# Performance work log

Measured on AMD Instinct MI355X. Metric: run time of the kernel, lower is better.

Reference implementation:

```python
import jax, jax.numpy as jnp
import numpy as np

THRESH = 0.5
MARGIN = 0.1
SCALE_POS = 2.0
SCALE_NEG = 40.0
EPS = 1e-5


def setup_inputs() -> dict:
    key = jax.random.key(0)
    k1, k2 = jax.random.split(key)
    B, D, NUM_CLASSES = 4096, 512, 512
    feats = jax.random.normal(k1, (B, D), dtype=jnp.float32)
    feats = feats / jnp.linalg.norm(feats, axis=1, keepdims=True)  # unit-norm embeddings
    labels = jax.random.randint(k2, (B,), 0, NUM_CLASSES, dtype=jnp.int64)
    return {"feats": feats, "labels": labels, "label_num": 26}


def reference(feats, labels, label_num):
    B = feats.shape[0]
    sim = feats @ feats.T  # [B, B]
    same = labels[:, None] == labels[None, :]
    pos_m = same & (sim < 1.0 - EPS)      # pos_pair_ mask per row
    neg_m = ~same                         # neg_pair_ mask per row
    has_pos = pos_m.any(axis=1)
    has_neg = neg_m.any(axis=1)
    min_pos = jnp.min(jnp.where(pos_m, sim, jnp.inf), axis=1)
    max_neg = jnp.max(jnp.where(neg_m, sim, -jnp.inf), axis=1)
    pos_thr = jnp.where(has_pos, min_pos, jnp.float32(0.2))  # fallback when no pos pairs
    neg_thr = jnp.where(has_neg, max_neg, jnp.float32(0.8))  # fallback when no neg pairs
    # mined pairs (same semantics as the per-row boolean filtering)
    neg_pair = neg_m & (sim + MARGIN > pos_thr[:, None])
    pos_pair = pos_m & (sim - MARGIN < neg_thr[:, None])
    valid = pos_pair.any(axis=1) & neg_pair.any(axis=1) & (jnp.arange(B) < B - label_num)
    # masked log-sum-exp style reductions (exp of -inf on masked entries -> 0)
    pos_sum = jnp.sum(jnp.exp(jnp.where(pos_pair, -SCALE_POS * (sim - THRESH), -jnp.inf)), axis=1)
    neg_sum = jnp.sum(jnp.exp(jnp.where(neg_pair, SCALE_NEG * (sim - THRESH), -jnp.inf)), axis=1)
    per_row = (1.0 / SCALE_POS) * jnp.log1p(pos_sum) + (1.0 / SCALE_NEG) * jnp.log1p(neg_sum)
    return jnp.sum(jnp.where(valid, per_row, 0.0)) / B
```

## Files before the change

kernel.cpp:

```cpp
#include <hip/hip_runtime.h>
#include <stdint.h>

#define BN 4096
#define DK 512
#define THRESH 0.5f
#define MARGIN 0.1f

typedef __attribute__((ext_vector_type(8))) __bf16 bf16x8;
typedef __attribute__((ext_vector_type(4))) float f32x4;
typedef __attribute__((ext_vector_type(8))) unsigned short ushort8;

__device__ __forceinline__ unsigned short f2bf(float f) {
    unsigned u = __float_as_uint(f);
    u += 0x7FFFu + ((u >> 16) & 1u);
    return (unsigned short)(u >> 16);
}
__device__ __forceinline__ float bf2f(unsigned short b) {
    return __uint_as_float((unsigned)b << 16);
}

__device__ __forceinline__ void async_cp16(void* lds, const void* g) {
    __builtin_amdgcn_global_load_lds(
        (const __attribute__((address_space(1))) void*)g,
        (__attribute__((address_space(3))) void*)lds,
        16, 0, 0);
}

__global__ void cvt_kernel(const float4* __restrict__ in, ushort4* __restrict__ out,
                           float* __restrict__ loss_out) {
    int i = blockIdx.x * blockDim.x + threadIdx.x;
    float4 v = in[i];
    ushort4 o;
    o.x = f2bf(v.x); o.y = f2bf(v.y); o.z = f2bf(v.z); o.w = f2bf(v.w);
    out[i] = o;
    if (blockIdx.x == 0 && threadIdx.x == 0) loss_out[0] = 0.f;
}

__global__ __launch_bounds__(256, 4) void ms_gemm(
    const unsigned short* __restrict__ Fb,
    unsigned short* __restrict__ simb)
{
    __shared__ __align__(16) unsigned short As[128 * 64];
    __shared__ __align__(16) unsigned short Bs[128 * 64];

    const int t    = threadIdx.x;
    const int lane = t & 63;
    const int w    = t >> 6;
    const int wr   = w >> 1, wc = w & 1;
    const int quad = lane >> 4;
    const int cIdx = lane & 15;

    const int rowBase = blockIdx.y * 128;
    const int colBase = blockIdx.x * 128;

    f32x4 acc[4][4];
#pragma unroll
    for (int i = 0; i < 4; ++i)
#pragma unroll
        for (int j = 0; j < 4; ++j) acc[i][j] = (f32x4){0.f, 0.f, 0.f, 0.f};

    const int lrow   = t >> 3;
    const int swz    = (t & 7) ^ (lrow & 7);
    const int ldsOff = t * 8;

    for (int k0 = 0; k0 < DK; k0 += 64) {
#pragma unroll
        for (int it = 0; it < 4; ++it) {
            const unsigned short* gA =
                Fb + (size_t)(rowBase + it * 32 + lrow) * DK + k0 + swz * 8;
            async_cp16(&As[it * 2048 + ldsOff], gA);
        }
#pragma unroll
        for (int it = 0; it < 4; ++it) {
            const unsigned short* gB =
                Fb + (size_t)(colBase + it * 32 + lrow) * DK + k0 + swz * 8;
            async_cp16(&Bs[it * 2048 + ldsOff], gB);
        }
        __syncthreads();

#pragma unroll
        for (int kk = 0; kk < 2; ++kk) {
            bf16x8 af[4], bg[4];
#pragma unroll
            for (int im = 0; im < 4; ++im) {
                int r = wr * 64 + im * 16 + cIdx;
                int p = (kk * 4 + quad) ^ (r & 7);
                af[im] = *reinterpret_cast<const bf16x8*>(&As[r * 64 + p * 8]);
            }
#pragma unroll
            for (int jn = 0; jn < 4; ++jn) {
                int c = wc * 64 + jn * 16 + cIdx;
                int p = (kk * 4 + quad) ^ (c & 7);
                bg[jn] = *reinterpret_cast<const bf16x8*>(&Bs[c * 64 + p * 8]);
            }
#pragma unroll
            for (int im = 0; im < 4; ++im)
#pragma unroll
                for (int jn = 0; jn < 4; ++jn)
                    acc[im][jn] = __builtin_amdgcn_mfma_f32_16x16x32_bf16(
                        af[im], bg[jn], acc[im][jn], 0, 0, 0);
        }
        __syncthreads();
    }

#pragma unroll
    for (int im = 0; im < 4; ++im)
#pragma unroll
        for (int rg = 0; rg < 4; ++rg) {
            const int grow = rowBase + wr * 64 + im * 16 + quad * 4 + rg;
            unsigned short* dst = simb + (size_t)grow * BN + colBase + wc * 64 + cIdx;
#pragma unroll
            for (int jn = 0; jn < 4; ++jn)
                dst[jn * 16] = f2bf(acc[im][jn][rg]);
        }
}

__global__ __launch_bounds__(256) void ms_rows(
    const unsigned short* __restrict__ simb,
    const int* __restrict__ labels,
    const int* __restrict__ label_num,
    float* __restrict__ out)
{
    __shared__ int   labS[BN];
    __shared__ float bsum[4];

    const int t    = threadIdx.x;
    const int lane = t & 63;
    const int w    = t >> 6;

    for (int i = t; i < BN; i += 256) labS[i] = labels[i];
    __syncthreads();

    const int lim = BN - label_num[0];
    float wsum = 0.f;

    for (int rr = 0; rr < 4; ++rr) {
        const int row = blockIdx.x * 16 + w * 4 + rr;
        const int lr  = labS[row];
        const ushort8* rp = (const ushort8*)(simb + (size_t)row * BN);

        ushort8 d[8];
        uint64_t mpos = 0, msame = 0;
        float mn = INFINITY, mx = -INFINITY;
#pragma unroll
        for (int j = 0; j < 8; ++j) {
            d[j] = rp[j * 64 + lane];
#pragma unroll
            for (int e = 0; e < 8; ++e) {
                const int col = (j * 64 + lane) * 8 + e;
                const float s = bf2f(d[j][e]);
                const bool same = (labS[col] == lr);
                const bool pos  = same && (col != row);
                if (pos)   mn = fminf(mn, s);
                if (!same) mx = fmaxf(mx, s);
                msame |= (uint64_t)same << (j * 8 + e);
                mpos  |= (uint64_t)pos  << (j * 8 + e);
            }
        }
#pragma unroll
        for (int off = 1; off < 64; off <<= 1) {
            mn = fminf(mn, __shfl_xor(mn, off, 64));
            mx = fmaxf(mx, __shfl_xor(mx, off, 64));
        }
        const float tP = (mn < 1e30f)  ? mn : 0.2f;
        const float tN = (mx > -1e30f) ? mx : 0.8f;

        float ps = 0.f, ns = 0.f;
#pragma unroll
        for (int j = 0; j < 8; ++j)
#pragma unroll
            for (int e = 0; e < 8; ++e) {
                const int k = j * 8 + e;
                const float s = bf2f(d[j][e]);
                if (((mpos >> k) & 1) && (s - MARGIN < tN))
                    ps += __expf(-2.0f * (s - THRESH));
                if (!((msame >> k) & 1) && (s + MARGIN > tP))
                    ns += __expf(40.0f * (s - THRESH));
            }
#pragma unroll
        for (int off = 1; off < 64; off <<= 1) {
            ps += __shfl_xor(ps, off, 64);
            ns += __shfl_xor(ns, off, 64);
        }
        if (lane == 0 && ps > 0.f && ns > 0.f && row < lim)
            wsum += 0.5f * log1pf(ps) + 0.025f * log1pf(ns);
    }

    if (lane == 0) bsum[w] = wsum;
    __syncthreads();
    if (t == 0)
        atomicAdd(out, (bsum[0] + bsum[1] + bsum[2] + bsum[3]) * (1.0f / (float)BN));
}

extern "C" void kernel_launch(void* const* d_in, const int* in_sizes, int n_in,
                              void* d_out, int out_size, void* d_ws, size_t ws_size,
                              hipStream_t stream)
{
    const float* feats     = (const float*)d_in[0];
    const int*   labels    = (const int*)d_in[1];
    const int*   label_num = (const int*)d_in[2];
    float*       out       = (float*)d_out;

    char* ws = (char*)d_ws;
    unsigned short* Fb   = (unsigned short*)ws;
    unsigned short* simb = (unsigned short*)(ws + 4u * 1024u * 1024u);

    cvt_kernel<<<2048, 256, 0, stream>>>((const float4*)feats, (ushort4*)Fb, out);

    dim3 grid(BN / 128, BN / 128);
    ms_gemm<<<grid, 256, 0, stream>>>(Fb, simb);

    ms_rows<<<256, 256, 0, stream>>>(simb, labels, label_num, out);
}
```

Baseline: 124.7 us.

## Exploit Gram matrix symmetry: compute upper-triangle tiles and mirror via LDS transpose

The GEMM now launches only the 528 upper-triangular 128x128 tiles of the symmetric F·F^T matrix. Each off-diagonal tile also writes its transpose through a swizzled LDS staging buffer, which nearly halves the MFMA work. The row-reduction kernel is also changed to one row per wave with 1024 blocks, for more parallelism. The cost is an extra LDS round trip and a second set of global writes per tile. Computing the tile index with a serial while-loop adds a small amount of scalar overhead.

```diff
diff --git a/kernel.cpp b/kernel.cpp
--- a/kernel.cpp
+++ b/kernel.cpp
@@ -40,8 +40,9 @@
     const unsigned short* __restrict__ Fb,
     unsigned short* __restrict__ simb)
 {
-    __shared__ __align__(16) unsigned short As[128 * 64];
-    __shared__ __align__(16) unsigned short Bs[128 * 64];
+    __shared__ __align__(16) unsigned short SMEM[2 * 128 * 64];
+    unsigned short* As = SMEM;
+    unsigned short* Bs = SMEM + 128 * 64;
 
     const int t    = threadIdx.x;
     const int lane = t & 63;
@@ -50,8 +51,11 @@
     const int quad = lane >> 4;
     const int cIdx = lane & 15;
 
-    const int rowBase = blockIdx.y * 128;
-    const int colBase = blockIdx.x * 128;
+    int l = blockIdx.x, by = 0;
+    while (l >= 32 - by) { l -= (32 - by); ++by; }
+    const int bx = by + l;
+    const int rowBase = by * 128;
+    const int colBase = bx * 128;
 
     f32x4 acc[4][4];
 #pragma unroll
@@ -113,6 +117,40 @@
             for (int jn = 0; jn < 4; ++jn)
                 dst[jn * 16] = f2bf(acc[im][jn][rg]);
         }
+
+    if (by == bx) return;
+
+#pragma unroll
+    for (int im = 0; im < 4; ++im)
+#pragma unroll
+        for (int jn = 0; jn < 4; ++jn) {
+            ushort4 v;
+            v.x = f2bf(acc[im][jn][0]);
+            v.y = f2bf(acc[im][jn][1]);
+            v.z = f2bf(acc[im][jn][2]);
+            v.w = f2bf(acc[im][jn][3]);
+            const int c  = wc * 64 + jn * 16 + cIdx;
+            const int r  = wr * 64 + im * 16 + quad * 4;
+            const int r8 = r >> 3;
+            const int ri = r & 7;
+            *reinterpret_cast<ushort4*>(
+                &SMEM[c * 128 + ((r8 ^ (c & 15)) << 3) + ri]) = v;
+        }
+    __syncthreads();
+
+    const int lch = t & 7;
+    const int trw = t >> 3;
+#pragma unroll
+    for (int it = 0; it < 4; ++it) {
+        const int tr = it * 32 + trw;
+        const int q1 = lch ^ (tr & 15);
+        const int q2 = (lch + 8) ^ (tr & 15);
+        ushort8 a = *reinterpret_cast<const ushort8*>(&SMEM[tr * 128 + q1 * 8]);
+        ushort8 b = *reinterpret_cast<const ushort8*>(&SMEM[tr * 128 + q2 * 8]);
+        unsigned short* dst = simb + (size_t)(colBase + tr) * BN + rowBase;
+        *reinterpret_cast<ushort8*>(&dst[lch * 8])       = a;
+        *reinterpret_cast<ushort8*>(&dst[(lch + 8) * 8]) = b;
+    }
 }
 
 __global__ __launch_bounds__(256) void ms_rows(
@@ -132,59 +170,56 @@
     __syncthreads();
 
     const int lim = BN - label_num[0];
+    const int row = blockIdx.x * 4 + w;
+    const int lr  = labS[row];
+    const ushort8* rp = (const ushort8*)(simb + (size_t)row * BN);
+
+    ushort8 d[8];
+    uint64_t mpos = 0, msame = 0;
+    float mn = INFINITY, mx = -INFINITY;
+#pragma unroll
+    for (int j = 0; j < 8; ++j) {
+        d[j] = rp[j * 64 + lane];
+#pragma unroll
+        for (int e = 0; e < 8; ++e) {
+            const int col = (j * 64 + lane) * 8 + e;
+            const float s = bf2f(d[j][e]);
+            const bool same = (labS[col] == lr);
+            const bool pos  = same && (col != row);
+            if (pos)   mn = fminf(mn, s);
+            if (!same) mx = fmaxf(mx, s);
+            msame |= (uint64_t)same << (j * 8 + e);
+            mpos  |= (uint64_t)pos  << (j * 8 + e);
+        }
+    }
+#pragma unroll
+    for (int off = 1; off < 64; off <<= 1) {
+        mn = fminf(mn, __shfl_xor(mn, off, 64));
+        mx = fmaxf(mx, __shfl_xor(mx, off, 64));
+    }
+    const float tP = (mn < 1e30f)  ? mn : 0.2f;
+    const float tN = (mx > -1e30f) ? mx : 0.8f;
+
+    float ps = 0.f, ns = 0.f;
+#pragma unroll
+    for (int j = 0; j < 8; ++j)
+#pragma unroll
+        for (int e = 0; e < 8; ++e) {
+            const int k = j * 8 + e;
+            const float s = bf2f(d[j][e]);
+            if (((mpos >> k) & 1) && (s - MARGIN < tN))
+                ps += __expf(-2.0f * (s - THRESH));
+            if (!((msame >> k) & 1) && (s + MARGIN > tP))
+                ns += __expf(40.0f * (s - THRESH));
+        }
+#pragma unroll
+    for (int off = 1; off < 64; off <<= 1) {
+        ps += __shfl_xor(ps, off, 64);
+        ns += __shfl_xor(ns, off, 64);
+    }
     float wsum = 0.f;
-
-    for (int rr = 0; rr < 4; ++rr) {
-        const int row = blockIdx.x * 16 + w * 4 + rr;
-        const int lr  = labS[row];
-        const ushort8* rp = (const ushort8*)(simb + (size_t)row * BN);
-
-        ushort8 d[8];
-        uint64_t mpos = 0, msame = 0;
-        float mn = INFINITY, mx = -INFINITY;
-#pragma unroll
-        for (int j = 0; j < 8; ++j) {
-            d[j] = rp[j * 64 + lane];
-#pragma unroll
-            for (int e = 0; e < 8; ++e) {
-                const int col = (j * 64 + lane) * 8 + e;
-                const float s = bf2f(d[j][e]);
-                const bool same = (labS[col] == lr);
-                const bool pos  = same && (col != row);
-                if (pos)   mn = fminf(mn, s);
-                if (!same) mx = fmaxf(mx, s);
-                msame |= (uint64_t)same << (j * 8 + e);
-                mpos  |= (uint64_t)pos  << (j * 8 + e);
-            }
-        }
-#pragma unroll
-        for (int off = 1; off < 64; off <<= 1) {
-            mn = fminf(mn, __shfl_xor(mn, off, 64));
-            mx = fmaxf(mx, __shfl_xor(mx, off, 64));
-        }
-        const float tP = (mn < 1e30f)  ? mn : 0.2f;
-        const float tN = (mx > -1e30f) ? mx : 0.8f;
-
-        float ps = 0.f, ns = 0.f;
-#pragma unroll
-        for (int j = 0; j < 8; ++j)
-#pragma unroll
-            for (int e = 0; e < 8; ++e) {
-                const int k = j * 8 + e;
-                const float s = bf2f(d[j][e]);
-                if (((mpos >> k) & 1) && (s - MARGIN < tN))
-                    ps += __expf(-2.0f * (s - THRESH));
-                if (!((msame >> k) & 1) && (s + MARGIN > tP))
-                    ns += __expf(40.0f * (s - THRESH));
-            }
-#pragma unroll
-        for (int off = 1; off < 64; off <<= 1) {
-            ps += __shfl_xor(ps, off, 64);
-            ns += __shfl_xor(ns, off, 64);
-        }
-        if (lane == 0 && ps > 0.f && ns > 0.f && row < lim)
-            wsum += 0.5f * log1pf(ps) + 0.025f * log1pf(ns);
-    }
+    if (lane == 0 && ps > 0.f && ns > 0.f && row < lim)
+        wsum = 0.5f * log1pf(ps) + 0.025f * log1pf(ns);
 
     if (lane == 0) bsum[w] = wsum;
     __syncthreads();
@@ -207,8 +242,7 @@
 
     cvt_kernel<<<2048, 256, 0, stream>>>((const float4*)feats, (ushort4*)Fb, out);
 
-    dim3 grid(BN / 128, BN / 128);
-    ms_gemm<<<grid, 256, 0, stream>>>(Fb, simb);
-
-    ms_rows<<<256, 256, 0, stream>>>(simb, labels, label_num, out);
-}
+    ms_gemm<<<528, 256, 0, stream>>>(Fb, simb);
+
+    ms_rows<<<1024, 256, 0, stream>>>(simb, labels, label_num, out);
+}
```

Measured after the change: 112.2 us. 1.11x faster.
